# Performance work log

Hardware: AMD Instinct MI355X
Metric: run time of the kernel (lower is better)

## Reference

```python
import jax, jax.numpy as jnp
import numpy as np

NUM_SKILLS = 1000
DIM_S = 64
SIZE_M = 64
B, T = 64, 200


def setup_inputs() -> dict:
    key = jax.random.key(0)
    ks = jax.random.split(key, 16)
    skills = jax.random.randint(ks[0], (B, T), 0, NUM_SKILLS)
    responses = jax.random.randint(ks[1], (B, T), 0, 2)
    s = 1.0 / np.sqrt(DIM_S)
    return {
        "skills": skills,
        "responses": responses,
        "k_emb": jax.random.normal(ks[2], (NUM_SKILLS, DIM_S)) * s,
        "v_emb": jax.random.normal(ks[3], (2 * NUM_SKILLS, DIM_S)) * s,
        "Mk": jax.random.normal(ks[4], (SIZE_M, DIM_S)) * np.sqrt(2.0 / DIM_S),
        "Mv0": jax.random.normal(ks[5], (SIZE_M, DIM_S)) * np.sqrt(2.0 / DIM_S),
        "fW": jax.random.normal(ks[6], (DIM_S, 2 * DIM_S)) * (1.0 / np.sqrt(2 * DIM_S)),
        "fb": jnp.zeros((DIM_S,)),
        "eW": jax.random.normal(ks[7], (DIM_S, DIM_S)) * s,
        "eb": jnp.zeros((DIM_S,)),
        "aW": jax.random.normal(ks[8], (DIM_S, DIM_S)) * s,
        "ab": jnp.zeros((DIM_S,)),
        "pW": jax.random.normal(ks[9], (1, DIM_S)) * s,
        "pb": jnp.zeros((1,)),
    }


def reference(skills, responses, k_emb, v_emb, Mk, Mv0, fW, fb, eW, eb, aW, ab, pW, pb):
    # dropout is identity in eval mode
    masked_r = responses * (responses > -1).astype(responses.dtype)
    x = skills + NUM_SKILLS * masked_r            # [B, T]
    k = k_emb[skills]                              # [B, T, D]
    v = v_emb[x]                                   # [B, T, D]
    w = jax.nn.softmax(jnp.einsum('btd,md->btm', k, Mk), axis=-1)  # [B, T, M]
    e = jax.nn.sigmoid(v @ eW.T + eb)              # [B, T, D]
    a = jnp.tanh(v @ aW.T + ab)                    # [B, T, D]

    Mv_init = jnp.broadcast_to(Mv0, (skills.shape[0],) + Mv0.shape)  # [B, M, D]

    def step(Mvt, inp):
        wt, et, at = inp                           # [B,M], [B,D], [B,D]
        read = jnp.einsum('bm,bmd->bd', wt, Mvt)   # read BEFORE update (Mv[:, :-1])
        Mvt = Mvt * (1.0 - wt[:, :, None] * et[:, None, :]) + wt[:, :, None] * at[:, None, :]
        return Mvt, read

    xs = (jnp.swapaxes(w, 0, 1), jnp.swapaxes(e, 0, 1), jnp.swapaxes(a, 0, 1))
    _, reads = jax.lax.scan(step, Mv_init, xs)     # reads: [T, B, D]
    reads = jnp.swapaxes(reads, 0, 1)              # [B, T, D]

    f = jnp.tanh(jnp.concatenate([reads, k], axis=-1) @ fW.T + fb)  # [B, T, D]
    p = jax.nn.sigmoid(f @ pW.T + pb)[..., 0]      # [B, T]
    return p[:, 1:]                                # pred, [B, T-1]
```

## Files before the change

kernel.cpp:

```cpp
#include <hip/hip_runtime.h>
#include <hip/hip_bf16.h>
#include <stdint.h>

#define NSK 1000
#define TT  200
#define BB  64
#define NROW (BB * TT)
#define NOUT (BB * (TT-1))
#define CH  20
#define RW  4

__device__ __forceinline__ float lane_bcast(float v, int l) {
  return __uint_as_float(__builtin_amdgcn_readlane(__float_as_uint(v), l));
}
__device__ __forceinline__ unsigned ulane_bcast(unsigned v, int l) {
  return __builtin_amdgcn_readlane(v, l);
}
__device__ __forceinline__ float frcp(float x) { return __builtin_amdgcn_rcpf(x); }
__device__ __forceinline__ float sigm(float x) { return frcp(1.f + __expf(-x)); }
__device__ __forceinline__ float tanh_fast(float x) {
  return fmaf(-2.f, frcp(1.f + __expf(2.f * x)), 1.f);
}

typedef _Float16 half2v __attribute__((ext_vector_type(2)));
union H2U { unsigned u; half2v h; };
__device__ __forceinline__ unsigned pack2h(float a, float b) {
  H2U x; x.h = (half2v){(_Float16)a, (_Float16)b}; return x.u;
}
__device__ __forceinline__ unsigned short f16bits(float x) {
  H2U u; u.h = (half2v){(_Float16)x, (_Float16)0.f}; return (unsigned short)(u.u & 0xffffu);
}
__device__ __forceinline__ float f16lo(unsigned bits) {
  H2U u; u.u = bits; return (float)u.h.x;
}
__device__ __forceinline__ float f16hi(unsigned bits) {
  H2U u; u.u = bits; return (float)u.h.y;
}
__device__ __forceinline__ float dot2h(unsigned sp, unsigned wp, float acc) {
#if __has_builtin(__builtin_amdgcn_fdot2)
  H2U s, w; s.u = sp; w.u = wp;
  return __builtin_amdgcn_fdot2(s.h, w.h, acc, false);
#else
  H2U s, w; s.u = sp; w.u = wp;
  return fmaf((float)s.h.y, (float)w.h.y, fmaf((float)s.h.x, (float)w.h.x, acc));
#endif
}
__device__ __forceinline__ unsigned pack_pairs(float v) {
  const int lane = threadIdx.x & 63;
  float a = __shfl(v, 2 * lane);
  float b = __shfl(v, 2 * lane + 1);
  return pack2h(a, b);
}

__global__ __launch_bounds__(256) void wea_kernel(
    const int* __restrict__ skills, const int* __restrict__ responses,
    const float* __restrict__ k_emb, const float* __restrict__ v_emb,
    const float* __restrict__ Mk, const float* __restrict__ eW,
    const float* __restrict__ eb, const float* __restrict__ aW,
    const float* __restrict__ ab,
    unsigned* __restrict__ ea_ws, unsigned short* __restrict__ w16_ws)
{
  __shared__ unsigned sw[3 * 64 * 40];
  const int tid = threadIdx.x;
  for (int ch = tid; ch < 1536; ch += 256) {
    const int mat = ch >> 9, rem = ch & 511;
    const int j = rem >> 3, cc = rem & 7;
    const float4* src = (mat == 0) ? (const float4*)Mk
                      : (mat == 1) ? (const float4*)eW : (const float4*)aW;
    const float4 f0 = src[j * 16 + cc * 2];
    const float4 f1 = src[j * 16 + cc * 2 + 1];
    uint4 pk;
    pk.x = pack2h(f0.x, f0.y); pk.y = pack2h(f0.z, f0.w);
    pk.z = pack2h(f1.x, f1.y); pk.w = pack2h(f1.z, f1.w);
    *(uint4*)&sw[mat * 2560 + j * 40 + ((cc + j) & 7) * 4] = pk;
  }
  __syncthreads();

  const int wave = tid >> 6, lane = tid & 63;
  const float ebl = eb[lane], abl = ab[lane];
  const int r0 = (blockIdx.x * 4 + wave) * 2;

  float kv[2], vv[2];
  #pragma unroll
  for (int i = 0; i < 2; ++i) {
    const int sk = skills[r0 + i];
    int rr = responses[r0 + i]; rr = (rr > -1) ? rr : 0;
    kv[i] = k_emb[(size_t)sk * 64 + lane];
    vv[i] = v_emb[(size_t)(sk + NSK * rr) * 64 + lane];
  }
  unsigned kp[2], vp[2];
  #pragma unroll
  for (int i = 0; i < 2; ++i) { kp[i] = pack_pairs(kv[i]); vp[i] = pack_pairs(vv[i]); }

  float accK[2] = {0.f, 0.f}, accE[2] = {0.f, 0.f}, accA[2] = {0.f, 0.f};
  #pragma unroll 1
  for (int h = 0; h < 2; ++h) {
    uint4 qm[4], qe[4], qa[4];
    #pragma unroll
    for (int c = 0; c < 4; ++c) {
      const int off = lane * 40 + (((h * 4 + c) + lane) & 7) * 4;
      qm[c] = *(const uint4*)&sw[off];
      qe[c] = *(const uint4*)&sw[2560 + off];
      qa[c] = *(const uint4*)&sw[5120 + off];
    }
    #pragma unroll
    for (int i = 0; i < 2; ++i) {
      #pragma unroll
      for (int c = 0; c < 4; ++c) {
        const unsigned um[4] = {qm[c].x, qm[c].y, qm[c].z, qm[c].w};
        const unsigned ue[4] = {qe[c].x, qe[c].y, qe[c].z, qe[c].w};
        const unsigned ua[4] = {qa[c].x, qa[c].y, qa[c].z, qa[c].w};
        #pragma unroll
        for (int m = 0; m < 4; ++m) {
          const int idx = (h * 4 + c) * 4 + m;
          const unsigned spk = ulane_bcast(kp[i], idx);
          const unsigned spv = ulane_bcast(vp[i], idx);
          accK[i] = dot2h(spk, um[m], accK[i]);
          accE[i] = dot2h(spv, ue[m], accE[i]);
          accA[i] = dot2h(spv, ua[m], accA[i]);
        }
      }
    }
  }
  #pragma unroll
  for (int i = 0; i < 2; ++i) {
    const int row = r0 + i;
    float mx = accK[i];
    #pragma unroll
    for (int off = 32; off; off >>= 1) mx = fmaxf(mx, __shfl_xor(mx, off));
    float ex = __expf(accK[i] - mx);
    float sm = ex;
    #pragma unroll
    for (int off = 32; off; off >>= 1) sm += __shfl_xor(sm, off);
    const float wv  = ex * frcp(sm);
    const float evv = sigm(accE[i] + ebl);
    const float avv = tanh_fast(accA[i] + abl);
    ea_ws[(size_t)row * 64 + lane]  = pack2h(evv, avv);
    w16_ws[(size_t)row * 64 + lane] = f16bits(wv);
  }
}

__device__ __forceinline__ void load_chunk(
    const unsigned* __restrict__ eap, const unsigned short* __restrict__ wp,
    int t0, int wl, int lane, unsigned* eab, unsigned* wvb)
{
  #pragma unroll
  for (int k = 0; k < CH; ++k) {
    eab[k] = eap[(t0 + k) * 64 + lane];
    wvb[k] = (unsigned)wp[(t0 + k) * 64 + wl];
  }
}

__device__ __forceinline__ void compute_chunk(
    float* Mv, const unsigned* eab, const unsigned* wvb,
    float* __restrict__ red, int wave, int lane)
{
  #pragma unroll
  for (int k = 0; k < CH; ++k) {
    const float ev = f16lo(eab[k]), av = f16hi(eab[k]);
    float rp = 0.f;
    #pragma unroll
    for (int i = 0; i < RW; ++i) {
      const float wm = f16lo(ulane_bcast(wvb[k], i));
      rp = fmaf(wm, Mv[i], rp);
      float tp = fmaf(-ev, Mv[i], av);
      Mv[i] = fmaf(wm, tp, Mv[i]);
    }
    red[k * 256 + wave * 64 + lane] = rp;
  }
}

__device__ __forceinline__ void reduce_store(
    const float* __restrict__ red, int ch, int base, int wave, int lane,
    unsigned short* __restrict__ ps)
{
  #pragma unroll
  for (int u = 0; u < 5; ++u) {
    const int k = wave * 5 + u;
    const float* rr = red + k * 256;
    const float v = (rr[lane] + rr[64 + lane]) + (rr[128 + lane] + rr[192 + lane]);
    ps[(size_t)(base + ch * CH + k) * 64 + lane] = f16bits(v);
  }
}

__global__ __launch_bounds__(256) void scan_kernel(
    const float* __restrict__ Mv0,
    const unsigned* __restrict__ ea_ws, const unsigned short* __restrict__ w16_ws,
    unsigned short* __restrict__ p0, unsigned short* __restrict__ p1,
    unsigned short* __restrict__ p2, unsigned short* __restrict__ p3)
{
  __shared__ float red[2][CH * 256];
  const int b    = blockIdx.x >> 2;
  const int s    = blockIdx.x & 3;
  const int wave = threadIdx.x >> 6;
  const int lane = threadIdx.x & 63;
  const int base = b * TT;
  const int m0   = s * 16 + wave * RW;
  const int wl   = m0 + (lane & (RW - 1));
  unsigned short* ps = (s == 0) ? p0 : (s == 1) ? p1 : (s == 2) ? p2 : p3;

  float Mv[RW];
  #pragma unroll
  for (int i = 0; i < RW; ++i) Mv[i] = Mv0[(size_t)(m0 + i) * 64 + lane];

  const unsigned* eap = ea_ws + (size_t)base * 64;
  const unsigned short* wp = w16_ws + (size_t)base * 64;

  unsigned ea0[CH], wv0[CH], ea1[CH], wv1[CH];
  load_chunk(eap, wp, 0, wl, lane, ea0, wv0);
  for (int ch = 0; ch < TT / CH; ch += 2) {
    if ((ch + 1) * CH < TT)
      load_chunk(eap, wp, (ch + 1) * CH, wl, lane, ea1, wv1);
    compute_chunk(Mv, ea0, wv0, red[0], wave, lane);
    __syncthreads();
    reduce_store(red[0], ch, base, wave, lane, ps);
    if ((ch + 2) * CH < TT)
      load_chunk(eap, wp, (ch + 2) * CH, wl, lane, ea0, wv0);
    if ((ch + 1) * CH < TT) {
      compute_chunk(Mv, ea1, wv1, red[1], wave, lane);
      __syncthreads();
      reduce_store(red[1], ch + 1, base, wave, lane, ps);
    }
  }
}

__global__ __launch_bounds__(256) void fp_kernel(
    const int* __restrict__ skills, const float* __restrict__ k_emb,
    const float* __restrict__ fW, const float* __restrict__ fb,
    const float* __restrict__ pW, const float* __restrict__ pb,
    const unsigned short* __restrict__ p0, const unsigned short* __restrict__ p1,
    const unsigned short* __restrict__ p2, const unsigned short* __restrict__ p3,
    float* __restrict__ out)
{
  __shared__ unsigned sf[64 * 72];
  const int tid = threadIdx.x;
  for (int ch = tid; ch < 1024; ch += 256) {
    const int j = ch >> 4, cc = ch & 15;
    const float4 f0 = ((const float4*)fW)[j * 32 + cc * 2];
    const float4 f1 = ((const float4*)fW)[j * 32 + cc * 2 + 1];
    uint4 pk;
    pk.x = pack2h(f0.x, f0.y); pk.y = pack2h(f0.z, f0.w);
    pk.z = pack2h(f1.x, f1.y); pk.w = pack2h(f1.z, f1.w);
    *(uint4*)&sf[j * 72 + ((cc + j) & 15) * 4] = pk;
  }
  __syncthreads();

  const int wave = tid >> 6, lane = tid & 63;
  const float fbl = fb[lane], pwl = pW[lane], pb0 = pb[0];
  const int p = blockIdx.x * 4 + wave;

  float rv[2], kc[2];
  int bsave[2], tsave[2];
  #pragma unroll
  for (int i = 0; i < 2; ++i) {
    const unsigned idx = 2u * p + i;
    const unsigned b = idx / 199u;
    const int row = (int)(idx + b + 1u);
    bsave[i] = (int)b; tsave[i] = (int)(idx - b * 199u);
    rv[i] = (f16lo((unsigned)p0[(size_t)row * 64 + lane])
           + f16lo((unsigned)p1[(size_t)row * 64 + lane]))
          + (f16lo((unsigned)p2[(size_t)row * 64 + lane])
           + f16lo((unsigned)p3[(size_t)row * 64 + lane]));
    kc[i] = k_emb[(size_t)skills[row] * 64 + lane];
  }
  unsigned rvp[2], kvp[2];
  #pragma unroll
  for (int i = 0; i < 2; ++i) {
    rvp[i] = pack_pairs(rv[i]);
    kvp[i] = pack_pairs(kc[i]);
  }

  float acc[2] = {fbl, fbl};
  #pragma unroll 1
  for (int h = 0; h < 4; ++h) {
    uint4 qf[4];
    #pragma unroll
    for (int c = 0; c < 4; ++c)
      qf[c] = *(const uint4*)&sf[lane * 72 + (((h * 4 + c) + lane) & 15) * 4];
    #pragma unroll
    for (int i = 0; i < 2; ++i) {
      #pragma unroll
      for (int c = 0; c < 4; ++c) {
        const unsigned uu[4] = {qf[c].x, qf[c].y, qf[c].z, qf[c].w};
        #pragma unroll
        for (int m = 0; m < 4; ++m) {
          const int idx = (h * 4 + c) * 4 + m;
          const unsigned sp = (idx < 32) ? ulane_bcast(rvp[i], idx)
                                         : ulane_bcast(kvp[i], idx - 32);
          acc[i] = dot2h(sp, uu[m], acc[i]);
        }
      }
    }
  }

  float f0 = tanh_fast(acc[0]) * pwl;
  float f1 = tanh_fast(acc[1]) * pwl;
  #pragma unroll
  for (int off = 32; off; off >>= 1) {
    f0 += __shfl_xor(f0, off);
    f1 += __shfl_xor(f1, off);
  }
  if (lane == 0) {
    out[(size_t)bsave[0] * (TT - 1) + tsave[0]] = sigm(f0 + pb0);
    out[(size_t)bsave[1] * (TT - 1) + tsave[1]] = sigm(f1 + pb0);
  }
}

extern "C" void kernel_launch(void* const* d_in, const int* in_sizes, int n_in,
                              void* d_out, int out_size, void* d_ws, size_t ws_size,
                              hipStream_t stream) {
  const int* skills    = (const int*)d_in[0];
  const int* responses = (const int*)d_in[1];
  const float* k_emb   = (const float*)d_in[2];
  const float* v_emb   = (const float*)d_in[3];
  const float* Mk      = (const float*)d_in[4];
  const float* Mv0     = (const float*)d_in[5];
  const float* fW      = (const float*)d_in[6];
  const float* fb      = (const float*)d_in[7];
  const float* eW      = (const float*)d_in[8];
  const float* eb      = (const float*)d_in[9];
  const float* aW      = (const float*)d_in[10];
  const float* ab      = (const float*)d_in[11];
  const float* pW      = (const float*)d_in[12];
  const float* pb      = (const float*)d_in[13];

  unsigned* ea_ws        = (unsigned*)d_ws;
  unsigned short* w16_ws = (unsigned short*)(ea_ws + (size_t)NROW * 64);
  unsigned short* p0     = w16_ws + (size_t)NROW * 64;
  unsigned short* p1     = p0 + (size_t)NROW * 64;
  unsigned short* p2     = p1 + (size_t)NROW * 64;
  unsigned short* p3     = p2 + (size_t)NROW * 64;

  wea_kernel<<<dim3(NROW / 8), 256, 0, stream>>>(
      skills, responses, k_emb, v_emb, Mk, eW, eb, aW, ab, ea_ws, w16_ws);
  scan_kernel<<<dim3(BB * 4), 256, 0, stream>>>(Mv0, ea_ws, w16_ws, p0, p1, p2, p3);
  fp_kernel<<<dim3(NOUT / 8), 256, 0, stream>>>(
      skills, k_emb, fW, fb, pW, pb, p0, p1, p2, p3, (float*)d_out);
}
```

Before: 126.2 us.

## Compute key/erase/add projections with MFMA 16x16x32 f16 instead of dot2 loops

Replaces the first kernel's per-lane fdot2/readlane loops, which stage the weights in LDS, with MFMA f16 matrix instructions. Each wave now handles a 16-row tile and reads its weight fragments straight from global memory, then does the softmax over memory slots with reductions inside each 16-lane group. This cuts the ALU and LDS work of the projection stage. It keeps the launch to 400 blocks of 128 threads, and the output stores become strided rather than coalesced per row.

```diff
diff --git a/kernel.cpp b/kernel.cpp
--- a/kernel.cpp
+++ b/kernel.cpp
@@ -1,5 +1,4 @@
 #include <hip/hip_runtime.h>
-#include <hip/hip_bf16.h>
 #include <stdint.h>
 
 #define NSK 1000
@@ -10,9 +9,6 @@
 #define CH  20
 #define RW  4
 
-__device__ __forceinline__ float lane_bcast(float v, int l) {
-  return __uint_as_float(__builtin_amdgcn_readlane(__float_as_uint(v), l));
-}
 __device__ __forceinline__ unsigned ulane_bcast(unsigned v, int l) {
   return __builtin_amdgcn_readlane(v, l);
 }
@@ -23,6 +19,8 @@
 }
 
 typedef _Float16 half2v __attribute__((ext_vector_type(2)));
+typedef _Float16 v8h __attribute__((ext_vector_type(8)));
+typedef float    v4f __attribute__((ext_vector_type(4)));
 union H2U { unsigned u; half2v h; };
 __device__ __forceinline__ unsigned pack2h(float a, float b) {
   H2U x; x.h = (half2v){(_Float16)a, (_Float16)b}; return x.u;
@@ -51,8 +49,12 @@
   float b = __shfl(v, 2 * lane + 1);
   return pack2h(a, b);
 }
-
-__global__ __launch_bounds__(256) void wea_kernel(
+__device__ __forceinline__ v8h pk8(float4 x0, float4 x1) {
+  return (v8h){(_Float16)x0.x, (_Float16)x0.y, (_Float16)x0.z, (_Float16)x0.w,
+               (_Float16)x1.x, (_Float16)x1.y, (_Float16)x1.z, (_Float16)x1.w};
+}
+
+__global__ __launch_bounds__(128) void wea_mfma(
     const int* __restrict__ skills, const int* __restrict__ responses,
     const float* __restrict__ k_emb, const float* __restrict__ v_emb,
     const float* __restrict__ Mk, const float* __restrict__ eW,
@@ -60,83 +62,84 @@
     const float* __restrict__ ab,
     unsigned* __restrict__ ea_ws, unsigned short* __restrict__ w16_ws)
 {
-  __shared__ unsigned sw[3 * 64 * 40];
-  const int tid = threadIdx.x;
-  for (int ch = tid; ch < 1536; ch += 256) {
-    const int mat = ch >> 9, rem = ch & 511;
-    const int j = rem >> 3, cc = rem & 7;
-    const float4* src = (mat == 0) ? (const float4*)Mk
-                      : (mat == 1) ? (const float4*)eW : (const float4*)aW;
-    const float4 f0 = src[j * 16 + cc * 2];
-    const float4 f1 = src[j * 16 + cc * 2 + 1];
-    uint4 pk;
-    pk.x = pack2h(f0.x, f0.y); pk.y = pack2h(f0.z, f0.w);
-    pk.z = pack2h(f1.x, f1.y); pk.w = pack2h(f1.z, f1.w);
-    *(uint4*)&sw[mat * 2560 + j * 40 + ((cc + j) & 7) * 4] = pk;
-  }
-  __syncthreads();
-
-  const int wave = tid >> 6, lane = tid & 63;
-  const float ebl = eb[lane], abl = ab[lane];
-  const int r0 = (blockIdx.x * 4 + wave) * 2;
-
-  float kv[2], vv[2];
-  #pragma unroll
-  for (int i = 0; i < 2; ++i) {
-    const int sk = skills[r0 + i];
-    int rr = responses[r0 + i]; rr = (rr > -1) ? rr : 0;
-    kv[i] = k_emb[(size_t)sk * 64 + lane];
-    vv[i] = v_emb[(size_t)(sk + NSK * rr) * 64 + lane];
-  }
-  unsigned kp[2], vp[2];
-  #pragma unroll
-  for (int i = 0; i < 2; ++i) { kp[i] = pack_pairs(kv[i]); vp[i] = pack_pairs(vv[i]); }
-
-  float accK[2] = {0.f, 0.f}, accE[2] = {0.f, 0.f}, accA[2] = {0.f, 0.f};
-  #pragma unroll 1
-  for (int h = 0; h < 2; ++h) {
-    uint4 qm[4], qe[4], qa[4];
+  const int tid  = threadIdx.x;
+  const int wv   = tid >> 6, lane = tid & 63;
+  const int tile = blockIdx.x * 2 + wv;
+  const int r0   = tile * 16;
+  const int lr   = lane & 15;
+  const int lg   = lane >> 4;
+
+  const int sk = skills[r0 + lr];
+  int rr = responses[r0 + lr]; rr = (rr > -1) ? rr : 0;
+  const int vrow = sk + NSK * rr;
+
+  const float4* kq = (const float4*)(k_emb + (size_t)sk * 64);
+  const float4* vq = (const float4*)(v_emb + (size_t)vrow * 64);
+  v8h ak[2], av[2];
+  #pragma unroll
+  for (int t = 0; t < 2; ++t) {
+    const int o = t * 8 + lg * 2;
+    ak[t] = pk8(kq[o], kq[o + 1]);
+    av[t] = pk8(vq[o], vq[o + 1]);
+  }
+
+  float ebv[4], abv[4];
+  #pragma unroll
+  for (int c = 0; c < 4; ++c) { ebv[c] = eb[16 * c + lr]; abv[c] = ab[16 * c + lr]; }
+
+  v4f acK[4], acE[4], acA[4];
+  #pragma unroll
+  for (int c = 0; c < 4; ++c) {
+    acK[c] = (v4f){0.f, 0.f, 0.f, 0.f};
+    acE[c] = (v4f){0.f, 0.f, 0.f, 0.f};
+    acA[c] = (v4f){0.f, 0.f, 0.f, 0.f};
+  }
+
+  #pragma unroll
+  for (int c = 0; c < 4; ++c) {
+    const float4* mq = (const float4*)(Mk + (size_t)(16 * c + lr) * 64);
+    const float4* eq = (const float4*)(eW + (size_t)(16 * c + lr) * 64);
+    const float4* aq = (const float4*)(aW + (size_t)(16 * c + lr) * 64);
+    #pragma unroll
+    for (int t = 0; t < 2; ++t) {
+      const int o = t * 8 + lg * 2;
+      const v8h bm = pk8(mq[o], mq[o + 1]);
+      const v8h be = pk8(eq[o], eq[o + 1]);
+      const v8h ba = pk8(aq[o], aq[o + 1]);
+      acK[c] = __builtin_amdgcn_mfma_f32_16x16x32_f16(ak[t], bm, acK[c], 0, 0, 0);
+      acE[c] = __builtin_amdgcn_mfma_f32_16x16x32_f16(av[t], be, acE[c], 0, 0, 0);
+      acA[c] = __builtin_amdgcn_mfma_f32_16x16x32_f16(av[t], ba, acA[c], 0, 0, 0);
+    }
+  }
+
+  float rs[4];
+  #pragma unroll
+  for (int q = 0; q < 4; ++q) {
+    float m = fmaxf(fmaxf(acK[0][q], acK[1][q]), fmaxf(acK[2][q], acK[3][q]));
+    #pragma unroll
+    for (int off = 8; off; off >>= 1) m = fmaxf(m, __shfl_xor(m, off));
+    float s = 0.f;
     #pragma unroll
     for (int c = 0; c < 4; ++c) {
-      const int off = lane * 40 + (((h * 4 + c) + lane) & 7) * 4;
-      qm[c] = *(const uint4*)&sw[off];
-      qe[c] = *(const uint4*)&sw[2560 + off];
-      qa[c] = *(const uint4*)&sw[5120 + off];
-    }
-    #pragma unroll
-    for (int i = 0; i < 2; ++i) {
-      #pragma unroll
-      for (int c = 0; c < 4; ++c) {
-        const unsigned um[4] = {qm[c].x, qm[c].y, qm[c].z, qm[c].w};
-        const unsigned ue[4] = {qe[c].x, qe[c].y, qe[c].z, qe[c].w};
-        const unsigned ua[4] = {qa[c].x, qa[c].y, qa[c].z, qa[c].w};
-        #pragma unroll
-        for (int m = 0; m < 4; ++m) {
-          const int idx = (h * 4 + c) * 4 + m;
-          const unsigned spk = ulane_bcast(kp[i], idx);
-          const unsigned spv = ulane_bcast(vp[i], idx);
-          accK[i] = dot2h(spk, um[m], accK[i]);
-          accE[i] = dot2h(spv, ue[m], accE[i]);
-          accA[i] = dot2h(spv, ua[m], accA[i]);
-        }
-      }
-    }
-  }
-  #pragma unroll
-  for (int i = 0; i < 2; ++i) {
-    const int row = r0 + i;
-    float mx = accK[i];
-    #pragma unroll
-    for (int off = 32; off; off >>= 1) mx = fmaxf(mx, __shfl_xor(mx, off));
-    float ex = __expf(accK[i] - mx);
-    float sm = ex;
-    #pragma unroll
-    for (int off = 32; off; off >>= 1) sm += __shfl_xor(sm, off);
-    const float wv  = ex * frcp(sm);
-    const float evv = sigm(accE[i] + ebl);
-    const float avv = tanh_fast(accA[i] + abl);
-    ea_ws[(size_t)row * 64 + lane]  = pack2h(evv, avv);
-    w16_ws[(size_t)row * 64 + lane] = f16bits(wv);
+      acK[c][q] = __expf(acK[c][q] - m);
+      s += acK[c][q];
+    }
+    #pragma unroll
+    for (int off = 8; off; off >>= 1) s += __shfl_xor(s, off);
+    rs[q] = frcp(s);
+  }
+
+  #pragma unroll
+  for (int c = 0; c < 4; ++c) {
+    const int j = 16 * c + lr;
+    #pragma unroll
+    for (int q = 0; q < 4; ++q) {
+      const int row = r0 + lg * 4 + q;
+      w16_ws[(size_t)row * 64 + j] = f16bits(acK[c][q] * rs[q]);
+      const float ev = sigm(acE[c][q] + ebv[c]);
+      const float avv = tanh_fast(acA[c][q] + abv[c]);
+      ea_ws[(size_t)row * 64 + j] = pack2h(ev, avv);
+    }
   }
 }
 
@@ -331,7 +334,7 @@
   unsigned short* p2     = p1 + (size_t)NROW * 64;
   unsigned short* p3     = p2 + (size_t)NROW * 64;
 
-  wea_kernel<<<dim3(NROW / 8), 256, 0, stream>>>(
+  wea_mfma<<<dim3(400), 128, 0, stream>>>(
       skills, responses, k_emb, v_emb, Mk, eW, eb, aW, ab, ea_ws, w16_ws);
   scan_kernel<<<dim3(BB * 4), 256, 0, stream>>>(Mv0, ea_ws, w16_ws, p0, p1, p2, p3);
   fp_kernel<<<dim3(NOUT / 8), 256, 0, stream>>>(
```

Measured after the change: 121.9 us. -3.4%, faster.
